# Performance work log

Hardware: AMD Instinct MI355X
Metric: run time of the kernel (lower is better)

## Reference

```python
import jax, jax.numpy as jnp
import numpy as np

NUM_ANGLES = 120
MAX_CONF = 100
FIELD = 50  # prot_field_size L


def setup_inputs() -> dict:
    key = jax.random.key(0)
    ks = jax.random.split(key, 4)
    B = 16
    return {
        "receptor": jax.random.normal(ks[0], (B, 1, FIELD, FIELD), jnp.float32),
        "ligand": jax.random.normal(ks[1], (B, 1, FIELD, FIELD), jnp.float32),
        "w_repr": jax.random.normal(ks[2], (2, 1, 3, 3), jnp.float32) * 0.3,
        "b_repr": jnp.zeros((2,), jnp.float32),
        "w_score": jax.random.normal(ks[3], (1, 4), jnp.float32) * 0.1,
        "b_score": jnp.zeros((1,), jnp.float32),
    }


def reference(receptor, ligand, w_repr, b_repr, w_score, b_score):
    B, _, H, W = receptor.shape  # H = W = FIELD

    # ---- scoring_model.repr : conv(1->2, SAME) + ReLU (stand-in for EQ repr net)
    def repr_net(x):
        y = jax.lax.conv_general_dilated(
            x, w_repr, (1, 1), "SAME", dimension_numbers=("NCHW", "OIHW", "NCHW"))
        return jax.nn.relu(y + b_repr[None, :, None, None])

    rec_feat = repr_net(receptor)  # (B,2,H,W)
    lig_feat = repr_net(ligand)    # (B,2,H,W)

    # ---- rotate: torch affine_grid + grid_sample (bilinear, align_corners=True, zero pad)
    ang = (2.0 * np.pi / NUM_ANGLES) * jnp.arange(NUM_ANGLES, dtype=jnp.float32)
    ca, sa = jnp.cos(ang), jnp.sin(ang)
    lin = jnp.linspace(-1.0, 1.0, H)
    gy, gx = jnp.meshgrid(lin, lin, indexing="ij")  # rows=y, cols=x
    # theta = [[c,-s,0],[s,c,0]] maps output coords -> input coords
    x_in = ca[:, None, None] * gx - sa[:, None, None] * gy  # (A,H,W)
    y_in = sa[:, None, None] * gx + ca[:, None, None] * gy
    px = (x_in + 1.0) * 0.5 * (W - 1)
    py = (y_in + 1.0) * 0.5 * (H - 1)
    x0 = jnp.floor(px).astype(jnp.int32); y0 = jnp.floor(py).astype(jnp.int32)
    x1 = x0 + 1; y1 = y0 + 1
    wx1 = px - x0; wx0 = 1.0 - wx1
    wy1 = py - y0; wy0 = 1.0 - wy1

    def tap(yi, xi, wgt):
        val = lig_feat[:, :, jnp.clip(yi, 0, H - 1), jnp.clip(xi, 0, W - 1)]  # (B,C,A,H,W)
        ok = ((yi >= 0) & (yi < H) & (xi >= 0) & (xi < W)).astype(lig_feat.dtype)
        return val * (wgt * ok)

    lig_rot = (tap(y0, x0, wy0 * wx0) + tap(y0, x1, wy0 * wx1)
               + tap(y1, x0, wy1 * wx0) + tap(y1, x1, wy1 * wx1))
    lig_rot = jnp.transpose(lig_rot, (2, 0, 1, 3, 4))  # (A,B,C,H,W)

    # ---- ProteinConv2D: FFT cross-correlation over all channel pairs, output 2L x 2L
    S = 2 * H
    pad = ((0, 0), (0, 0), (0, H), (0, W))
    Frec = jnp.fft.rfft2(jnp.pad(rec_feat, pad))              # (B,C,S,S/2+1)
    Flig = jnp.fft.rfft2(jnp.pad(lig_rot, ((0, 0),) + pad))   # (A,B,C,S,S/2+1)
    cross = jnp.einsum("bcxy,abdxy->abcdxy", jnp.conj(Frec), Flig)
    A_, C = NUM_ANGLES, rec_feat.shape[1]
    corr = jnp.fft.irfft2(cross.reshape(A_, B, C * C, S, S // 2 + 1), s=(S, S))
    corr = jnp.fft.fftshift(corr, axes=(-2, -1))              # (A,B,4,S,S) centered

    # ---- scoring_model.scorer : Linear(4->1) applied per translation
    scores = jnp.einsum("abcij,c->abij", corr, w_score[0]) + b_score[0]  # (A,B,S,S)

    # ---- update_top: greedy iterative argmin extraction with zero masking
    flat = scores.reshape(A_, B, S * S)

    def greedy(v):
        def step(s, _):
            i = jnp.argmin(s)
            return s.at[i].set(0.0), (i, s[i])
        _, (idx, val) = jax.lax.scan(step, v, None, length=MAX_CONF)
        return idx, val

    idxs, vals = jax.vmap(jax.vmap(greedy))(flat)  # each (A,B,K)

    # ---- final top-1 per batch over all angles/extractions (stable first-min tiebreak)
    K = MAX_CONF
    vals_b = jnp.transpose(vals, (1, 0, 2)).reshape(B, A_ * K)
    j = jnp.argmin(vals_b, axis=1)
    a = j // K
    k = j % K
    pos = idxs[a, jnp.arange(B), k]
    Lf = jnp.float32(S / 2)
    x = (pos // S).astype(jnp.float32)
    y = (pos % S).astype(jnp.float32)
    angles_out = ang[a][:, None]                               # (B,1)
    translations = jnp.stack([x - Lf, y - Lf], axis=1)         # (B,2)
    return angles_out, translations
```

## Files before the change

### kernel.cpp

```cpp
#include <hip/hip_runtime.h>
#include <math.h>

#define NANG 120
#define NB   16
#define H    50
#define SD   100
#define NBIN 51
#define PADB 7
#define BROWS 69
#define BST  106
#define WST  104
#define RTST 52
#define CLAG 100
#define AX   58

__device__ __align__(16) float g_Arec[NB*2*AX*NBIN*2 + 64];
__device__ __align__(16) float g_ligc[NB*2*H*H];
__device__ __align__(16) float g_W[H*WST];
__device__ __align__(16) float g_P[NBIN*128 + 64];
__device__ __align__(16) float g_C[(size_t)NANG*NB*5100];
__device__ unsigned long long g_key[NB];

__device__ const int g_s8[8][2] = {
  {-1,127},{-9,47},{7,-49},{-17,39},{15,-41},{-25,31},{23,-33},{127,127}
};

__global__ __launch_bounds__(512) void k_prep(const float* __restrict__ rec,
                                              const float* __restrict__ lig,
                                              const float* __restrict__ wr,
                                              const float* __restrict__ br,
                                              const float* __restrict__ wsc) {
  const int blk = blockIdx.x;
  const int tid = threadIdx.x;
  if (blk == NB*4) {
    for (int u = tid; u < H*WST; u += 512) {
      int y = u / WST, col = u % WST;
      float v = 0.f;
      if (col < 2*NBIN) {
        int om = col >> 1;
        int k = (om * y) % SD;
        double ang = 6.283185307179586 * (double)k / 100.0;
        v = (col & 1) ? (float)(-sin(ang)) : (float)cos(ang);
      }
      g_W[u] = v;
    }
    for (int u = tid; u < NBIN*128; u += 512) {
      int om = u >> 7, q = u & 127;
      int dy = q >> 1;
      float v = 0.f;
      if (dy <= 49) {
        int k = (om * dy) % SD;
        double ang = 6.283185307179586 * (double)k / 100.0;
        v = (q & 1) ? (float)sin(ang) : (float)cos(ang);
      }
      g_P[u] = v;
    }
    for (int i = tid; i < NB; i += 512) g_key[i] = (0x80000000ULL << 21);
    return;
  }
  const int b = blk >> 2;
  const int part = blk & 3;
  const int omBase = part * 13;
  const int nOm = (part == 3) ? 12 : 13;
  __shared__ float recf[2*H*H];
  __shared__ float tbl[SD*2];
  for (int k = tid; k < SD; k += 512) {
    double ang = 6.283185307179586 * (double)k / 100.0;
    tbl[2*k]   = (float)cos(ang);
    tbl[2*k+1] = (float)sin(ang);
  }
  const float* rimg = rec + b*H*H;
  const float* limg = lig + b*H*H;
  for (int p = tid; p < H*H; p += 512) {
    int i = p / H, j = p - (p/H)*H;
    float ar0 = br[0], ar1 = br[1], al0 = br[0], al1 = br[1];
    for (int di = 0; di < 3; ++di) {
      int ii = i + di - 1;
      if (ii < 0 || ii >= H) continue;
      for (int dj = 0; dj < 3; ++dj) {
        int jj = j + dj - 1;
        if (jj < 0 || jj >= H) continue;
        float rv = rimg[ii*H+jj], lv = limg[ii*H+jj];
        float w0 = wr[di*3 + dj], w1 = wr[9 + di*3 + dj];
        ar0 += w0*rv; ar1 += w1*rv; al0 += w0*lv; al1 += w1*lv;
      }
    }
    ar0 = fmaxf(ar0, 0.f); ar1 = fmaxf(ar1, 0.f);
    recf[p] = ar0; recf[H*H + p] = ar1;
    if (part == 0) {
      al0 = fmaxf(al0, 0.f); al1 = fmaxf(al1, 0.f);
      g_ligc[((b*2+0)*H + i)*H + j] = wsc[0]*al0 + wsc[1]*al1;
      g_ligc[((b*2+1)*H + i)*H + j] = wsc[2]*al0 + wsc[3]*al1;
    }
  }
  if (part == 0) {
    for (int u = tid; u < 2*8*102; u += 512) {
      int c = u / 816; int r = u % 816;
      int x = 50 + r / 102; int q = r % 102;
      g_Arec[((b*2+c)*AX + x)*102 + q] = 0.f;
    }
  }
  __syncthreads();
  for (int u = tid; u < 2*H*nOm; u += 512) {
    int om = omBase + u % nOm;
    int rest = u / nOm; int x = rest % H; int c = rest / H;
    const float* row = recf + (c*H + x)*H;
    float sr = 0.f, si = 0.f;
    int k = 0;
    for (int y = 0; y < H; ++y) {
      float rv = row[y];
      sr += rv * tbl[2*k];
      si -= rv * tbl[2*k+1];
      k += om; if (k >= SD) k -= SD;
    }
    float* dst = g_Arec + ((b*2+c)*AX + x)*102 + 2*om;
    dst[0] = sr; dst[1] = si;
  }
}

#define STEP8(uu) do { \
  float Ar = ar_[(uu)&7], Ai = ai_[(uu)&7]; \
  { const int sl=(uu)&7;     cr0 += Ar*br_[sl]+Ai*bi_[sl]; ci0 += Ar*bi_[sl]-Ai*br_[sl]; } \
  { const int sl=((uu)+1)&7; cr1 += Ar*br_[sl]+Ai*bi_[sl]; ci1 += Ar*bi_[sl]-Ai*br_[sl]; } \
  { const int sl=((uu)+2)&7; cr2 += Ar*br_[sl]+Ai*bi_[sl]; ci2 += Ar*bi_[sl]-Ai*br_[sl]; } \
  { const int sl=((uu)+3)&7; cr3 += Ar*br_[sl]+Ai*bi_[sl]; ci3 += Ar*bi_[sl]-Ai*br_[sl]; } \
  { const int sl=((uu)+4)&7; cr4 += Ar*br_[sl]+Ai*bi_[sl]; ci4 += Ar*bi_[sl]-Ai*br_[sl]; } \
  { const int sl=((uu)+5)&7; cr5 += Ar*br_[sl]+Ai*bi_[sl]; ci5 += Ar*bi_[sl]-Ai*br_[sl]; } \
  { const int sl=((uu)+6)&7; cr6 += Ar*br_[sl]+Ai*bi_[sl]; ci6 += Ar*bi_[sl]-Ai*br_[sl]; } \
  { const int sl=((uu)+7)&7; cr7 += Ar*br_[sl]+Ai*bi_[sl]; ci7 += Ar*bi_[sl]-Ai*br_[sl]; } \
} while(0)

#define TILE8(D0) do { \
  const int d0 = (D0); \
  const int x_lo = max(0, -(d0+7)); \
  const int x_hi = min(H, H - d0); \
  const int ng = (x_hi - x_lo + 7) >> 3; \
  float cr0=0,cr1=0,cr2=0,cr3=0,cr4=0,cr5=0,cr6=0,cr7=0; \
  float ci0=0,ci1=0,ci2=0,ci3=0,ci4=0,ci5=0,ci6=0,ci7=0; \
  _Pragma("unroll 1") \
  for (int c = 0; c < 2; ++c) { \
    const float* Ap = g_Arec + ((b*2+c)*AX + x_lo)*102 + 2*om; \
    const float* Bp = sB + c*(BROWS*BST) + (PADB + x_lo + d0)*BST + 2*om; \
    float br_[8], bi_[8], ar_[8], ai_[8]; \
    _Pragma("unroll") \
    for (int s = 0; s < 8; ++s) { \
      float2 bv = *(const float2*)&Bp[s*BST]; \
      br_[s] = bv.x; bi_[s] = bv.y; \
      float2 av = *(const float2*)&Ap[s*102]; \
      ar_[s] = av.x; ai_[s] = av.y; \
    } \
    _Pragma("unroll 1") \
    for (int g = 0; g < ng-1; ++g) { \
      _Pragma("unroll") \
      for (int u = 0; u < 8; ++u) { \
        STEP8(u); \
        float2 bv = *(const float2*)&Bp[(u+8)*BST]; \
        br_[u] = bv.x; bi_[u] = bv.y; \
        float2 av = *(const float2*)&Ap[(u+8)*102]; \
        ar_[u] = av.x; ai_[u] = av.y; \
      } \
      Bp += 8*BST; Ap += 8*102; \
    } \
    _Pragma("unroll") \
    for (int u = 0; u < 8; ++u) { \
      STEP8(u); \
      if (u < 7) { \
        float2 bv = *(const float2*)&Bp[(u+8)*BST]; \
        br_[u] = bv.x; bi_[u] = bv.y; \
      } \
    } \
  } \
  if (omValid) { \
    const float sc = (om == 0 || om == 50) ? 0.5f : 1.0f; \
    const int base = om*CLAG + (d0 + 49); \
    float* crl = CrL + base; \
    float* gci = g_C + (size_t)bid*5100 + base; \
    float4 v0 = {cr0*sc, cr1*sc, cr2*sc, cr3*sc}; \
    float4 w0 = {ci0*sc, ci1*sc, ci2*sc, ci3*sc}; \
    *(float4*)&crl[0] = v0; \
    *(float4*)&gci[0] = w0; \
    if (d0 != 47) { \
      float4 v1 = {cr4*sc, cr5*sc, cr6*sc, cr7*sc}; \
      float4 w1 = {ci4*sc, ci5*sc, ci6*sc, ci7*sc}; \
      *(float4*)&crl[4] = v1; \
      *(float4*)&gci[4] = w1; \
    } \
  } \
} while(0)

__global__ __launch_bounds__(512, 4) void k_main() {
  const int bid = blockIdx.x;
  const int a = bid % NANG;
  const int b = bid / NANG;
  const int tid = threadIdx.x;

  __shared__ __align__(16) float sMem[19828];
  float* sB  = sMem;
  float* Rt0 = sMem + 14628;
  float* Rt1 = sMem + 17228;
  float* CrL = sMem + 14628;
  float* CiL = sMem;
  float* sP  = sMem + 5100;

  for (int u = tid; u < 2*19*BST; u += 512) {
    int ch = u / (19*BST);
    int r  = (u % (19*BST)) / BST;
    int col = u % BST;
    int row = (r < PADB) ? r : r + 50;
    sB[ch*(BROWS*BST) + row*BST + col] = 0.f;
  }

  float angf = 0.05235987755982988f * (float)a;
  float ca = cosf(angf), sa = sinf(angf);
  const float* L0 = g_ligc + (b*2+0)*H*H;
  const float* L1 = g_ligc + (b*2+1)*H*H;
  for (int p = tid; p < H*H; p += 512) {
    int i = p / H, j = p - (p/H)*H;
    float gy = -1.f + (float)i*(2.f/49.f);
    float gx = -1.f + (float)j*(2.f/49.f);
    float x_in = ca*gx - sa*gy;
    float y_in = sa*gx + ca*gy;
    float px = (x_in + 1.f)*0.5f*49.f;
    float py = (y_in + 1.f)*0.5f*49.f;
    float fx = floorf(px), fy = floorf(py);
    int x0 = (int)fx, y0 = (int)fy;
    int x1 = x0 + 1, y1 = y0 + 1;
    float wx1 = px - fx, wx0 = 1.f - wx1;
    float wy1 = py - fy, wy0 = 1.f - wy1;
    float v0 = 0.f, v1 = 0.f;
    if (y0 >= 0 && y0 < H) {
      if (x0 >= 0 && x0 < H) { float w = wy0*wx0; int o = y0*H+x0; v0 += w*L0[o]; v1 += w*L1[o]; }
      if (x1 >= 0 && x1 < H) { float w = wy0*wx1; int o = y0*H+x1; v0 += w*L0[o]; v1 += w*L1[o]; }
    }
    if (y1 >= 0 && y1 < H) {
      if (x0 >= 0 && x0 < H) { float w = wy1*wx0; int o = y1*H+x0; v0 += w*L0[o]; v1 += w*L1[o]; }
      if (x1 >= 0 && x1 < H) { float w = wy1*wx1; int o = y1*H+x1; v0 += w*L0[o]; v1 += w*L1[o]; }
    }
    Rt0[j*RTST + i] = v0;
    Rt1[j*RTST + i] = v1;
  }
  __syncthreads();

  if (tid < 442) {
    int c = tid / 221;
    int r = tid % 221;
    int cg = r % 17;
    int it = r / 17;
    int i0 = it*4;
    int col0 = 6*cg;
    float pacc[4][6];
    #pragma unroll
    for (int p = 0; p < 4; ++p)
      #pragma unroll
      for (int q = 0; q < 6; ++q) pacc[p][q] = 0.f;
    const float* rtc = Rt0 + c*(H*RTST) + i0;
    const float* wt = g_W + col0;
    #pragma unroll 2
    for (int y = 0; y < H; ++y) {
      float4 rv = *(const float4*)&rtc[y*RTST];
      float ww[6];
      #pragma unroll
      for (int q = 0; q < 3; ++q) {
        float2 w2 = *(const float2*)&wt[y*WST + 2*q];
        ww[2*q] = w2.x; ww[2*q+1] = w2.y;
      }
      float rr[4] = {rv.x, rv.y, rv.z, rv.w};
      #pragma unroll
      for (int p = 0; p < 4; ++p)
        #pragma unroll
        for (int q = 0; q < 6; ++q) pacc[p][q] += rr[p]*ww[q];
    }
    float* dst = sB + c*(BROWS*BST) + col0;
    #pragma unroll
    for (int p = 0; p < 4; ++p) {
      int i = i0 + p;
      if (i < H) {
        #pragma unroll
        for (int q = 0; q < 3; ++q) {
          float2 o = {pacc[p][2*q], pacc[p][2*q+1]};
          *(float2*)&dst[(PADB+i)*BST + 2*q] = o;
        }
      }
    }
  }
  __syncthreads();

  const int wid = tid >> 6, lane = tid & 63;
  const int om = (lane <= 50) ? lane : 50;
  const bool omValid = (lane <= 50);
  const int d0A = g_s8[wid][0];
  const int d0B = g_s8[wid][1];

  if (d0A != 127) { TILE8(d0A); }
  if (d0B != 127) { TILE8(d0B); }
  __syncthreads();

  {
    const float4* src = (const float4*)(g_C + (size_t)bid*5100);
    float4* dst = (float4*)CiL;
    for (int u = tid; u < 1275; u += 512) dst[u] = src[u];
    for (int u = tid; u < 51*50; u += 512) {
      int o = u / 50, q2 = (u % 50)*2;
      *(float2*)&sP[o*100 + q2] = *(const float2*)&g_P[o*128 + q2];
    }
  }
  __syncthreads();

  float bestV = 3.0e38f; int bestP = 0;
  if (tid < 425) {
    int lt = tid % 25;
    int dt = tid / 25;
    int l0 = 4*lt, dy0 = 3*dt;
    float su[4][3], sv[4][3];
    #pragma unroll
    for (int k = 0; k < 4; ++k)
      #pragma unroll
      for (int j = 0; j < 3; ++j) { su[k][j] = 0.f; sv[k][j] = 0.f; }
    const float* crp = CrL + l0;
    const float* cip = CiL + l0;
    const float* tp = sP + 2*dy0;
    #pragma unroll 3
    for (int om2 = 0; om2 < NBIN; ++om2) {
      float4 c4 = *(const float4*)&crp[om2*CLAG];
      float4 i4 = *(const float4*)&cip[om2*CLAG];
      float2 t0 = *(const float2*)&tp[om2*100];
      float2 t1 = *(const float2*)&tp[om2*100 + 2];
      float2 t2 = *(const float2*)&tp[om2*100 + 4];
      float cc[4] = {c4.x, c4.y, c4.z, c4.w};
      float ii[4] = {i4.x, i4.y, i4.z, i4.w};
      float co[3] = {t0.x, t1.x, t2.x};
      float si[3] = {t0.y, t1.y, t2.y};
      #pragma unroll
      for (int k = 0; k < 4; ++k)
        #pragma unroll
        for (int j = 0; j < 3; ++j) {
          su[k][j] += cc[k]*co[j];
          sv[k][j] += ii[k]*si[j];
        }
    }
    #pragma unroll
    for (int k = 0; k < 4; ++k) {
      int lagIdx = l0 + k;
      if (lagIdx <= 98) {
        int row = lagIdx + 1;
        #pragma unroll
        for (int j = 0; j < 3; ++j) {
          int dy = dy0 + j;
          if (dy <= 49) {
            float vp = su[k][j] - sv[k][j];
            float vm = su[k][j] + sv[k][j];
            int posp = row*SD + (50 + dy);
            int posm = row*SD + (50 - dy);
            if (vp < bestV || (vp == bestV && posp < bestP)) { bestV = vp; bestP = posp; }
            if (vm < bestV || (vm == bestV && posm < bestP)) { bestV = vm; bestP = posm; }
          }
        }
      }
    }
  }

  #pragma unroll
  for (int off = 32; off > 0; off >>= 1) {
    float v2 = __shfl_xor(bestV, off, 64);
    int   p2 = __shfl_xor(bestP, off, 64);
    if (v2 < bestV || (v2 == bestV && p2 < bestP)) { bestV = v2; bestP = p2; }
  }
  if (lane == 0) {
    unsigned int u = __float_as_uint(bestV);
    u = (u & 0x80000000u) ? ~u : (u | 0x80000000u);
    unsigned long long key = ((unsigned long long)u << 21) |
                             ((unsigned long long)(unsigned)a << 14) |
                             (unsigned long long)(unsigned)bestP;
    atomicMin(&g_key[b], key);
  }
}

__global__ void k_final(float* __restrict__ out) {
  int b = threadIdx.x;
  if (b >= NB) return;
  unsigned long long key = g_key[b];
  int a   = (int)((key >> 14) & 127ULL);
  int pos = (int)(key & 16383ULL);
  out[b] = 0.05235987755982988f * (float)a;
  out[NB + 2*b]     = (float)(pos / SD) - 50.f;
  out[NB + 2*b + 1] = (float)(pos % SD) - 50.f;
}

extern "C" void kernel_launch(void* const* d_in, const int* in_sizes, int n_in,
                              void* d_out, int out_size, void* d_ws, size_t ws_size,
                              hipStream_t stream) {
  const float* rec = (const float*)d_in[0];
  const float* lig = (const float*)d_in[1];
  const float* wr  = (const float*)d_in[2];
  const float* br  = (const float*)d_in[3];
  const float* wsc = (const float*)d_in[4];
  (void)in_sizes; (void)n_in; (void)out_size; (void)d_ws; (void)ws_size;
  hipLaunchKernelGGL(k_prep, dim3(NB*4+1), dim3(512), 0, stream, rec, lig, wr, br, wsc);
  hipLaunchKernelGGL(k_main, dim3(NANG*NB), dim3(512), 0, stream);
  hipLaunchKernelGGL(k_final, dim3(1), dim3(64), 0, stream, (float*)d_out);
}
```

Before: 279.3 us.

## Shrink correlation lag tiles from 8 to 4 and rebalance per-wave lag slots

The per-wave correlation inner loop now accumulates 4 lags per tile instead of 8, with a new static table giving each of the 8 waves up to 5 lag slots for a more even triangular workload. Lag padding in the shared B buffer shrinks from 7 to 3 rows, cutting LDS footprint. This halves accumulator registers and reduces wasted work on short-overlap lags. In exchange, each A/B load feeds half as many FMAs, so loads per flop roughly double.

```diff
diff --git a/kernel.cpp b/kernel.cpp
--- a/kernel.cpp
+++ b/kernel.cpp
@@ -6,8 +6,8 @@
 #define H    50
 #define SD   100
 #define NBIN 51
-#define PADB 7
-#define BROWS 69
+#define PADB 3
+#define BROWS 63
 #define BST  106
 #define WST  104
 #define RTST 52
@@ -21,8 +21,15 @@
 __device__ __align__(16) float g_C[(size_t)NANG*NB*5100];
 __device__ unsigned long long g_key[NB];
 
-__device__ const int g_s8[8][2] = {
-  {-1,127},{-9,47},{7,-49},{-17,39},{15,-41},{-25,31},{23,-33},{127,127}
+__device__ const int g_s4[8][5] = {
+  { -1,-25,-49,127,127},
+  { -9, -5,127,127,127},
+  {  3,  7,127,127,127},
+  {-17,-13,-41,127,127},
+  { 11, 15,-37,127,127},
+  {-21, 19,-33,127,127},
+  { 23,-29, 35,-45,127},
+  { 27, 31, 39, 43, 47}
 };
 
 __global__ __launch_bounds__(512) void k_prep(const float* __restrict__ rec,
@@ -118,74 +125,12 @@
   }
 }
 
-#define STEP8(uu) do { \
+#define STEP4(uu) do { \
   float Ar = ar_[(uu)&7], Ai = ai_[(uu)&7]; \
   { const int sl=(uu)&7;     cr0 += Ar*br_[sl]+Ai*bi_[sl]; ci0 += Ar*bi_[sl]-Ai*br_[sl]; } \
   { const int sl=((uu)+1)&7; cr1 += Ar*br_[sl]+Ai*bi_[sl]; ci1 += Ar*bi_[sl]-Ai*br_[sl]; } \
   { const int sl=((uu)+2)&7; cr2 += Ar*br_[sl]+Ai*bi_[sl]; ci2 += Ar*bi_[sl]-Ai*br_[sl]; } \
   { const int sl=((uu)+3)&7; cr3 += Ar*br_[sl]+Ai*bi_[sl]; ci3 += Ar*bi_[sl]-Ai*br_[sl]; } \
-  { const int sl=((uu)+4)&7; cr4 += Ar*br_[sl]+Ai*bi_[sl]; ci4 += Ar*bi_[sl]-Ai*br_[sl]; } \
-  { const int sl=((uu)+5)&7; cr5 += Ar*br_[sl]+Ai*bi_[sl]; ci5 += Ar*bi_[sl]-Ai*br_[sl]; } \
-  { const int sl=((uu)+6)&7; cr6 += Ar*br_[sl]+Ai*bi_[sl]; ci6 += Ar*bi_[sl]-Ai*br_[sl]; } \
-  { const int sl=((uu)+7)&7; cr7 += Ar*br_[sl]+Ai*bi_[sl]; ci7 += Ar*bi_[sl]-Ai*br_[sl]; } \
-} while(0)
-
-#define TILE8(D0) do { \
-  const int d0 = (D0); \
-  const int x_lo = max(0, -(d0+7)); \
-  const int x_hi = min(H, H - d0); \
-  const int ng = (x_hi - x_lo + 7) >> 3; \
-  float cr0=0,cr1=0,cr2=0,cr3=0,cr4=0,cr5=0,cr6=0,cr7=0; \
-  float ci0=0,ci1=0,ci2=0,ci3=0,ci4=0,ci5=0,ci6=0,ci7=0; \
-  _Pragma("unroll 1") \
-  for (int c = 0; c < 2; ++c) { \
-    const float* Ap = g_Arec + ((b*2+c)*AX + x_lo)*102 + 2*om; \
-    const float* Bp = sB + c*(BROWS*BST) + (PADB + x_lo + d0)*BST + 2*om; \
-    float br_[8], bi_[8], ar_[8], ai_[8]; \
-    _Pragma("unroll") \
-    for (int s = 0; s < 8; ++s) { \
-      float2 bv = *(const float2*)&Bp[s*BST]; \
-      br_[s] = bv.x; bi_[s] = bv.y; \
-      float2 av = *(const float2*)&Ap[s*102]; \
-      ar_[s] = av.x; ai_[s] = av.y; \
-    } \
-    _Pragma("unroll 1") \
-    for (int g = 0; g < ng-1; ++g) { \
-      _Pragma("unroll") \
-      for (int u = 0; u < 8; ++u) { \
-        STEP8(u); \
-        float2 bv = *(const float2*)&Bp[(u+8)*BST]; \
-        br_[u] = bv.x; bi_[u] = bv.y; \
-        float2 av = *(const float2*)&Ap[(u+8)*102]; \
-        ar_[u] = av.x; ai_[u] = av.y; \
-      } \
-      Bp += 8*BST; Ap += 8*102; \
-    } \
-    _Pragma("unroll") \
-    for (int u = 0; u < 8; ++u) { \
-      STEP8(u); \
-      if (u < 7) { \
-        float2 bv = *(const float2*)&Bp[(u+8)*BST]; \
-        br_[u] = bv.x; bi_[u] = bv.y; \
-      } \
-    } \
-  } \
-  if (omValid) { \
-    const float sc = (om == 0 || om == 50) ? 0.5f : 1.0f; \
-    const int base = om*CLAG + (d0 + 49); \
-    float* crl = CrL + base; \
-    float* gci = g_C + (size_t)bid*5100 + base; \
-    float4 v0 = {cr0*sc, cr1*sc, cr2*sc, cr3*sc}; \
-    float4 w0 = {ci0*sc, ci1*sc, ci2*sc, ci3*sc}; \
-    *(float4*)&crl[0] = v0; \
-    *(float4*)&gci[0] = w0; \
-    if (d0 != 47) { \
-      float4 v1 = {cr4*sc, cr5*sc, cr6*sc, cr7*sc}; \
-      float4 w1 = {ci4*sc, ci5*sc, ci6*sc, ci7*sc}; \
-      *(float4*)&crl[4] = v1; \
-      *(float4*)&gci[4] = w1; \
-    } \
-  } \
 } while(0)
 
 __global__ __launch_bounds__(512, 4) void k_main() {
@@ -194,17 +139,17 @@
   const int b = bid / NANG;
   const int tid = threadIdx.x;
 
-  __shared__ __align__(16) float sMem[19828];
+  __shared__ __align__(16) float sMem[18556];
   float* sB  = sMem;
-  float* Rt0 = sMem + 14628;
-  float* Rt1 = sMem + 17228;
-  float* CrL = sMem + 14628;
+  float* Rt0 = sMem + 13356;
+  float* Rt1 = sMem + 15956;
+  float* CrL = sMem + 13356;
   float* CiL = sMem;
   float* sP  = sMem + 5100;
 
-  for (int u = tid; u < 2*19*BST; u += 512) {
-    int ch = u / (19*BST);
-    int r  = (u % (19*BST)) / BST;
+  for (int u = tid; u < 2*13*BST; u += 512) {
+    int ch = u / (13*BST);
+    int r  = (u % (13*BST)) / BST;
     int col = u % BST;
     int row = (r < PADB) ? r : r + 50;
     sB[ch*(BROWS*BST) + row*BST + col] = 0.f;
@@ -288,11 +233,57 @@
   const int wid = tid >> 6, lane = tid & 63;
   const int om = (lane <= 50) ? lane : 50;
   const bool omValid = (lane <= 50);
-  const int d0A = g_s8[wid][0];
-  const int d0B = g_s8[wid][1];
-
-  if (d0A != 127) { TILE8(d0A); }
-  if (d0B != 127) { TILE8(d0B); }
+
+  #pragma unroll 1
+  for (int slot = 0; slot < 5; ++slot) {
+    const int d0 = g_s4[wid][slot];
+    if (d0 == 127) continue;
+    const int x_lo = max(0, -(d0+3));
+    const int x_hi = min(H, H - d0);
+    const int ng = (x_hi - x_lo + 7) >> 3;
+    float cr0=0,cr1=0,cr2=0,cr3=0, ci0=0,ci1=0,ci2=0,ci3=0;
+    #pragma unroll 1
+    for (int c = 0; c < 2; ++c) {
+      const float* Ap = g_Arec + ((b*2+c)*AX + x_lo)*102 + 2*om;
+      const float* Bp = sB + c*(BROWS*BST) + (PADB + x_lo + d0)*BST + 2*om;
+      float br_[8], bi_[8], ar_[8], ai_[8];
+      #pragma unroll
+      for (int s = 0; s < 8; ++s) {
+        float2 bv = *(const float2*)&Bp[s*BST];
+        br_[s] = bv.x; bi_[s] = bv.y;
+        float2 av = *(const float2*)&Ap[s*102];
+        ar_[s] = av.x; ai_[s] = av.y;
+      }
+      #pragma unroll 1
+      for (int g = 0; g < ng-1; ++g) {
+        #pragma unroll
+        for (int u = 0; u < 8; ++u) {
+          STEP4(u);
+          float2 bv = *(const float2*)&Bp[(u+8)*BST];
+          br_[u] = bv.x; bi_[u] = bv.y;
+          float2 av = *(const float2*)&Ap[(u+8)*102];
+          ar_[u] = av.x; ai_[u] = av.y;
+        }
+        Bp += 8*BST; Ap += 8*102;
+      }
+      #pragma unroll
+      for (int u = 0; u < 8; ++u) {
+        STEP4(u);
+        if (u < 3) {
+          float2 bv = *(const float2*)&Bp[(u+8)*BST];
+          br_[u] = bv.x; bi_[u] = bv.y;
+        }
+      }
+    }
+    if (omValid) {
+      const float sc = (om == 0 || om == 50) ? 0.5f : 1.0f;
+      const int base = om*CLAG + (d0 + 49);
+      float4 v0 = {cr0*sc, cr1*sc, cr2*sc, cr3*sc};
+      float4 w0 = {ci0*sc, ci1*sc, ci2*sc, ci3*sc};
+      *(float4*)&CrL[base] = v0;
+      *(float4*)&(g_C + (size_t)bid*5100)[base] = w0;
+    }
+  }
   __syncthreads();
 
   {
```

After: 287.7 us. +3.0%, slower.

## Split main kernel into per-channel correlation kernel and separate reduction/argmin kernel

Applied to the files above, without the earlier changes.

The fused per-(angle,batch) kernel is split into k_corr, launched with one block per (angle,batch,channel), and k_p4, which sums the two channel partial spectra and runs the inverse-transform argmin. Shared memory per correlation block roughly halves and the grid doubles, aiming for higher occupancy and more parallelism. The partial results are now written to global memory as interleaved complex data and read back by a second launch. This adds an extra kernel launch and roughly doubles global traffic for the intermediate spectra.

```diff
diff --git a/kernel.cpp b/kernel.cpp
--- a/kernel.cpp
+++ b/kernel.cpp
@@ -8,17 +8,17 @@
 #define NBIN 51
 #define PADB 7
 #define BROWS 69
-#define BST  106
+#define BST  102
 #define WST  104
 #define RTST 52
-#define CLAG 100
+#define CST2 208
 #define AX   58
 
 __device__ __align__(16) float g_Arec[NB*2*AX*NBIN*2 + 64];
 __device__ __align__(16) float g_ligc[NB*2*H*H];
 __device__ __align__(16) float g_W[H*WST];
 __device__ __align__(16) float g_P[NBIN*128 + 64];
-__device__ __align__(16) float g_C[(size_t)NANG*NB*5100];
+__device__ __align__(64) float g_C[(size_t)NANG*NB*2*NBIN*CST2];
 __device__ unsigned long long g_key[NB];
 
 __device__ const int g_s8[8][2] = {
@@ -137,83 +137,69 @@
   const int ng = (x_hi - x_lo + 7) >> 3; \
   float cr0=0,cr1=0,cr2=0,cr3=0,cr4=0,cr5=0,cr6=0,cr7=0; \
   float ci0=0,ci1=0,ci2=0,ci3=0,ci4=0,ci5=0,ci6=0,ci7=0; \
+  const float* Ap = g_Arec + ((b*2+c)*AX + x_lo)*102 + 2*om; \
+  const float* Bp = sB + (PADB + x_lo + d0)*BST + 2*om; \
+  float br_[8], bi_[8], ar_[8], ai_[8]; \
+  _Pragma("unroll") \
+  for (int s = 0; s < 8; ++s) { \
+    float2 bv = *(const float2*)&Bp[s*BST]; \
+    br_[s] = bv.x; bi_[s] = bv.y; \
+    float2 av = *(const float2*)&Ap[s*102]; \
+    ar_[s] = av.x; ai_[s] = av.y; \
+  } \
   _Pragma("unroll 1") \
-  for (int c = 0; c < 2; ++c) { \
-    const float* Ap = g_Arec + ((b*2+c)*AX + x_lo)*102 + 2*om; \
-    const float* Bp = sB + c*(BROWS*BST) + (PADB + x_lo + d0)*BST + 2*om; \
-    float br_[8], bi_[8], ar_[8], ai_[8]; \
-    _Pragma("unroll") \
-    for (int s = 0; s < 8; ++s) { \
-      float2 bv = *(const float2*)&Bp[s*BST]; \
-      br_[s] = bv.x; bi_[s] = bv.y; \
-      float2 av = *(const float2*)&Ap[s*102]; \
-      ar_[s] = av.x; ai_[s] = av.y; \
-    } \
-    _Pragma("unroll 1") \
-    for (int g = 0; g < ng-1; ++g) { \
-      _Pragma("unroll") \
-      for (int u = 0; u < 8; ++u) { \
-        STEP8(u); \
-        float2 bv = *(const float2*)&Bp[(u+8)*BST]; \
-        br_[u] = bv.x; bi_[u] = bv.y; \
-        float2 av = *(const float2*)&Ap[(u+8)*102]; \
-        ar_[u] = av.x; ai_[u] = av.y; \
-      } \
-      Bp += 8*BST; Ap += 8*102; \
-    } \
+  for (int g = 0; g < ng-1; ++g) { \
     _Pragma("unroll") \
     for (int u = 0; u < 8; ++u) { \
       STEP8(u); \
-      if (u < 7) { \
-        float2 bv = *(const float2*)&Bp[(u+8)*BST]; \
-        br_[u] = bv.x; bi_[u] = bv.y; \
-      } \
+      float2 bv = *(const float2*)&Bp[(u+8)*BST]; \
+      br_[u] = bv.x; bi_[u] = bv.y; \
+      float2 av = *(const float2*)&Ap[(u+8)*102]; \
+      ar_[u] = av.x; ai_[u] = av.y; \
+    } \
+    Bp += 8*BST; Ap += 8*102; \
+  } \
+  _Pragma("unroll") \
+  for (int u = 0; u < 8; ++u) { \
+    STEP8(u); \
+    if (u < 7) { \
+      float2 bv = *(const float2*)&Bp[(u+8)*BST]; \
+      br_[u] = bv.x; bi_[u] = bv.y; \
     } \
   } \
   if (omValid) { \
     const float sc = (om == 0 || om == 50) ? 0.5f : 1.0f; \
-    const int base = om*CLAG + (d0 + 49); \
-    float* crl = CrL + base; \
-    float* gci = g_C + (size_t)bid*5100 + base; \
-    float4 v0 = {cr0*sc, cr1*sc, cr2*sc, cr3*sc}; \
-    float4 w0 = {ci0*sc, ci1*sc, ci2*sc, ci3*sc}; \
-    *(float4*)&crl[0] = v0; \
-    *(float4*)&gci[0] = w0; \
-    if (d0 != 47) { \
-      float4 v1 = {cr4*sc, cr5*sc, cr6*sc, cr7*sc}; \
-      float4 w1 = {ci4*sc, ci5*sc, ci6*sc, ci7*sc}; \
-      *(float4*)&crl[4] = v1; \
-      *(float4*)&gci[4] = w1; \
-    } \
+    float* dst = g_C + (size_t)bid2*(NBIN*CST2) + om*CST2 + (d0 + 49)*2; \
+    float4 q0 = {cr0*sc, ci0*sc, cr1*sc, ci1*sc}; \
+    float4 q1 = {cr2*sc, ci2*sc, cr3*sc, ci3*sc}; \
+    float4 q2 = {cr4*sc, ci4*sc, cr5*sc, ci5*sc}; \
+    float4 q3 = {cr6*sc, ci6*sc, cr7*sc, ci7*sc}; \
+    *(float4*)&dst[0]  = q0; *(float4*)&dst[4]  = q1; \
+    *(float4*)&dst[8]  = q2; *(float4*)&dst[12] = q3; \
   } \
 } while(0)
 
-__global__ __launch_bounds__(512, 4) void k_main() {
-  const int bid = blockIdx.x;
-  const int a = bid % NANG;
-  const int b = bid / NANG;
+__global__ __launch_bounds__(512, 4) void k_corr() {
+  const int bid2 = blockIdx.x;
+  const int idx = bid2 >> 1;
+  const int c = bid2 & 1;
+  const int a = idx % NANG;
+  const int b = idx / NANG;
   const int tid = threadIdx.x;
 
-  __shared__ __align__(16) float sMem[19828];
-  float* sB  = sMem;
-  float* Rt0 = sMem + 14628;
-  float* Rt1 = sMem + 17228;
-  float* CrL = sMem + 14628;
-  float* CiL = sMem;
-  float* sP  = sMem + 5100;
-
-  for (int u = tid; u < 2*19*BST; u += 512) {
-    int ch = u / (19*BST);
-    int r  = (u % (19*BST)) / BST;
-    int col = u % BST;
+  __shared__ __align__(16) float sMem[9638];
+  float* sB = sMem;
+  float* Rt = sMem + 7038;
+
+  for (int u = tid; u < 19*BST; u += 512) {
+    int r = u / BST;
     int row = (r < PADB) ? r : r + 50;
-    sB[ch*(BROWS*BST) + row*BST + col] = 0.f;
+    sB[row*BST + (u % BST)] = 0.f;
   }
 
   float angf = 0.05235987755982988f * (float)a;
   float ca = cosf(angf), sa = sinf(angf);
-  const float* L0 = g_ligc + (b*2+0)*H*H;
-  const float* L1 = g_ligc + (b*2+1)*H*H;
+  const float* Lc = g_ligc + (b*2+c)*H*H;
   for (int p = tid; p < H*H; p += 512) {
     int i = p / H, j = p - (p/H)*H;
     float gy = -1.f + (float)i*(2.f/49.f);
@@ -227,59 +213,54 @@
     int x1 = x0 + 1, y1 = y0 + 1;
     float wx1 = px - fx, wx0 = 1.f - wx1;
     float wy1 = py - fy, wy0 = 1.f - wy1;
-    float v0 = 0.f, v1 = 0.f;
+    float v = 0.f;
     if (y0 >= 0 && y0 < H) {
-      if (x0 >= 0 && x0 < H) { float w = wy0*wx0; int o = y0*H+x0; v0 += w*L0[o]; v1 += w*L1[o]; }
-      if (x1 >= 0 && x1 < H) { float w = wy0*wx1; int o = y0*H+x1; v0 += w*L0[o]; v1 += w*L1[o]; }
+      if (x0 >= 0 && x0 < H) v += (wy0*wx0)*Lc[y0*H+x0];
+      if (x1 >= 0 && x1 < H) v += (wy0*wx1)*Lc[y0*H+x1];
     }
     if (y1 >= 0 && y1 < H) {
-      if (x0 >= 0 && x0 < H) { float w = wy1*wx0; int o = y1*H+x0; v0 += w*L0[o]; v1 += w*L1[o]; }
-      if (x1 >= 0 && x1 < H) { float w = wy1*wx1; int o = y1*H+x1; v0 += w*L0[o]; v1 += w*L1[o]; }
-    }
-    Rt0[j*RTST + i] = v0;
-    Rt1[j*RTST + i] = v1;
+      if (x0 >= 0 && x0 < H) v += (wy1*wx0)*Lc[y1*H+x0];
+      if (x1 >= 0 && x1 < H) v += (wy1*wx1)*Lc[y1*H+x1];
+    }
+    Rt[j*RTST + i] = v;
   }
   __syncthreads();
 
-  if (tid < 442) {
-    int c = tid / 221;
-    int r = tid % 221;
-    int cg = r % 17;
-    int it = r / 17;
-    int i0 = it*4;
+  if (tid < 425) {
+    int cg = tid % 17;
+    int rp = tid / 17;
+    int i0 = 2*rp;
     int col0 = 6*cg;
-    float pacc[4][6];
+    float pacc[2][6];
     #pragma unroll
-    for (int p = 0; p < 4; ++p)
+    for (int p = 0; p < 2; ++p)
       #pragma unroll
       for (int q = 0; q < 6; ++q) pacc[p][q] = 0.f;
-    const float* rtc = Rt0 + c*(H*RTST) + i0;
+    const float* rtc = Rt + i0;
     const float* wt = g_W + col0;
     #pragma unroll 2
     for (int y = 0; y < H; ++y) {
-      float4 rv = *(const float4*)&rtc[y*RTST];
+      float2 rv = *(const float2*)&rtc[y*RTST];
       float ww[6];
       #pragma unroll
       for (int q = 0; q < 3; ++q) {
         float2 w2 = *(const float2*)&wt[y*WST + 2*q];
         ww[2*q] = w2.x; ww[2*q+1] = w2.y;
       }
-      float rr[4] = {rv.x, rv.y, rv.z, rv.w};
-      #pragma unroll
-      for (int p = 0; p < 4; ++p)
+      float rr[2] = {rv.x, rv.y};
+      #pragma unroll
+      for (int p = 0; p < 2; ++p)
         #pragma unroll
         for (int q = 0; q < 6; ++q) pacc[p][q] += rr[p]*ww[q];
     }
-    float* dst = sB + c*(BROWS*BST) + col0;
     #pragma unroll
-    for (int p = 0; p < 4; ++p) {
+    for (int p = 0; p < 2; ++p) {
       int i = i0 + p;
-      if (i < H) {
-        #pragma unroll
-        for (int q = 0; q < 3; ++q) {
-          float2 o = {pacc[p][2*q], pacc[p][2*q+1]};
-          *(float2*)&dst[(PADB+i)*BST + 2*q] = o;
-        }
+      float* dst = sB + (PADB + i)*BST + col0;
+      #pragma unroll
+      for (int q = 0; q < 3; ++q) {
+        float2 o = {pacc[p][2*q], pacc[p][2*q+1]};
+        *(float2*)&dst[2*q] = o;
       }
     }
   }
@@ -293,15 +274,24 @@
 
   if (d0A != 127) { TILE8(d0A); }
   if (d0B != 127) { TILE8(d0B); }
-  __syncthreads();
+}
+
+__global__ __launch_bounds__(512) void k_p4() {
+  const int bid = blockIdx.x;
+  const int a = bid % NANG;
+  const int b = bid / NANG;
+  const int tid = threadIdx.x;
+
+  __shared__ __align__(16) float CL[NBIN*CST2];
 
   {
-    const float4* src = (const float4*)(g_C + (size_t)bid*5100);
-    float4* dst = (float4*)CiL;
-    for (int u = tid; u < 1275; u += 512) dst[u] = src[u];
-    for (int u = tid; u < 51*50; u += 512) {
-      int o = u / 50, q2 = (u % 50)*2;
-      *(float2*)&sP[o*100 + q2] = *(const float2*)&g_P[o*128 + q2];
+    const float4* s0 = (const float4*)(g_C + (size_t)(bid*2+0)*(NBIN*CST2));
+    const float4* s1 = (const float4*)(g_C + (size_t)(bid*2+1)*(NBIN*CST2));
+    float4* d = (float4*)CL;
+    for (int u = tid; u < (NBIN*CST2)/4; u += 512) {
+      float4 x = s0[u], y = s1[u];
+      float4 z = {x.x+y.x, x.y+y.y, x.z+y.z, x.w+y.w};
+      d[u] = z;
     }
   }
   __syncthreads();
@@ -316,18 +306,17 @@
     for (int k = 0; k < 4; ++k)
       #pragma unroll
       for (int j = 0; j < 3; ++j) { su[k][j] = 0.f; sv[k][j] = 0.f; }
-    const float* crp = CrL + l0;
-    const float* cip = CiL + l0;
-    const float* tp = sP + 2*dy0;
+    const float* clp = CL + l0*2;
+    const float* tp = g_P + 2*dy0;
     #pragma unroll 3
     for (int om2 = 0; om2 < NBIN; ++om2) {
-      float4 c4 = *(const float4*)&crp[om2*CLAG];
-      float4 i4 = *(const float4*)&cip[om2*CLAG];
-      float2 t0 = *(const float2*)&tp[om2*100];
-      float2 t1 = *(const float2*)&tp[om2*100 + 2];
-      float2 t2 = *(const float2*)&tp[om2*100 + 4];
-      float cc[4] = {c4.x, c4.y, c4.z, c4.w};
-      float ii[4] = {i4.x, i4.y, i4.z, i4.w};
+      float4 a4 = *(const float4*)&clp[om2*CST2];
+      float4 b4 = *(const float4*)&clp[om2*CST2 + 4];
+      float2 t0 = *(const float2*)&tp[om2*128];
+      float2 t1 = *(const float2*)&tp[om2*128 + 2];
+      float2 t2 = *(const float2*)&tp[om2*128 + 4];
+      float cc[4] = {a4.x, a4.z, b4.x, b4.z};
+      float ii[4] = {a4.y, a4.w, b4.y, b4.w};
       float co[3] = {t0.x, t1.x, t2.x};
       float si[3] = {t0.y, t1.y, t2.y};
       #pragma unroll
@@ -365,7 +354,7 @@
     int   p2 = __shfl_xor(bestP, off, 64);
     if (v2 < bestV || (v2 == bestV && p2 < bestP)) { bestV = v2; bestP = p2; }
   }
-  if (lane == 0) {
+  if ((tid & 63) == 0) {
     unsigned int u = __float_as_uint(bestV);
     u = (u & 0x80000000u) ? ~u : (u | 0x80000000u);
     unsigned long long key = ((unsigned long long)u << 21) |
@@ -396,6 +385,7 @@
   const float* wsc = (const float*)d_in[4];
   (void)in_sizes; (void)n_in; (void)out_size; (void)d_ws; (void)ws_size;
   hipLaunchKernelGGL(k_prep, dim3(NB*4+1), dim3(512), 0, stream, rec, lig, wr, br, wsc);
-  hipLaunchKernelGGL(k_main, dim3(NANG*NB), dim3(512), 0, stream);
+  hipLaunchKernelGGL(k_corr, dim3(2*NANG*NB), dim3(512), 0, stream);
+  hipLaunchKernelGGL(k_p4,   dim3(NANG*NB), dim3(512), 0, stream);
   hipLaunchKernelGGL(k_final, dim3(1), dim3(64), 0, stream, (float*)d_out);
 }
```

Result: slower. 426.4 us (+52.7%).
